# Optimization experiments

Hardware: AMD Instinct MI355X
Metric: run time of the kernel (lower is better)

## Reference

```python
import jax, jax.numpy as jnp
import numpy as np

LENGTH = 512
Q = 2 * LENGTH + 3   # match + insert + flank/unannotated/terminal states
S = 26               # amino-acid alphabet size


def setup_inputs() -> dict:
    key = jax.random.key(0)
    k1, k2, k3, k4 = jax.random.split(key, 4)
    seq = jax.random.randint(k1, (256, 512), 0, S, dtype=jnp.int32)
    A_logits = jax.random.normal(k2, (Q, Q), dtype=jnp.float32)
    B_logits = jax.random.normal(k3, (Q, S), dtype=jnp.float32)
    init_logits = jax.random.normal(k4, (Q,), dtype=jnp.float32)
    return {"seq": seq, "A_logits": A_logits, "B_logits": B_logits,
            "init_logits": init_logits}


def reference(seq, A_logits, B_logits, init_logits):
    # Row-stochastic transition matrix A [q,q], emission matrix B [q,s],
    # initial state distribution init [q] (cell builds these from kernels
    # via softmax/normalization in make_A()/make_B()).
    A = jax.nn.softmax(A_logits, axis=-1)
    B = jax.nn.softmax(B_logits, axis=-1)
    init = jax.nn.softmax(init_logits)

    # Emission likelihoods per timestep: E[b,t,q] = B[q, seq[b,t]]
    E = B.T[seq]  # [batch, T, q]

    # Scaled HMM forward recursion (log-sum-exp in scaled prob space).
    alpha0 = init[None, :] * E[:, 0]            # [batch, q]
    s0 = jnp.sum(alpha0, axis=-1)               # [batch]
    carry0 = (alpha0 / s0[:, None], jnp.log(s0))

    def step(carry, e_t):
        alpha, ll = carry
        f = (alpha @ A) * e_t                   # [batch, q]
        s = jnp.sum(f, axis=-1)                 # scaling factor
        return (f / s[:, None], ll + jnp.log(s)), None

    E_rest = jnp.transpose(E[:, 1:], (1, 0, 2))  # [T-1, batch, q]
    (alpha, loglik), _ = jax.lax.scan(step, carry0, E_rest)
    return loglik  # per-sequence log-likelihood [batch]
```

## Files before the change

kernel.cpp:

```cpp
#include <hip/hip_runtime.h>
#include <math.h>

typedef __bf16 bf16x8 __attribute__((ext_vector_type(8)));
typedef float f32x4 __attribute__((ext_vector_type(4)));
typedef unsigned int u32x4 __attribute__((ext_vector_type(4)));
typedef unsigned long long u64;

constexpr int QQ = 1027;
constexpr int SS = 26;
constexpr int TT = 512;
constexpr int NB = 256;
constexpr int KP = 1056;
constexpr int NP = 1040;
constexpr int BTS = 1040;
constexpr int NSL = 13;
constexpr int NBB = 16;
constexpr int MB = 16;
constexpr int NWV = 5;
constexpr int CBLK = NWV * 64;
constexpr int KSTEPS = KP / 32;
constexpr int BUFN = NB * KP;
constexpr int RQ = KP / 4;
constexpr int LQ = 274;
constexpr int TOTQ = MB * RQ;
constexpr int NLD = TOTQ / CBLK;
constexpr int NREM = TOTQ - NLD * CBLK;
constexpr int NTAG = NSL * NWV;
constexpr int TSTR = 80;

__device__ __forceinline__ unsigned short f2bf(float f) {
  union { float f; unsigned u; } v; v.f = f;
  return (unsigned short)((v.u + 0x7fffu + ((v.u >> 16) & 1u)) >> 16);
}

__device__ __forceinline__ u64 ald8(const u64* p) {
  return __hip_atomic_load((u64*)p, __ATOMIC_RELAXED, __HIP_MEMORY_SCOPE_AGENT);
}
__device__ __forceinline__ void ast8(u64* p, u64 v) {
  __hip_atomic_store(p, v, __ATOMIC_RELAXED, __HIP_MEMORY_SCOPE_AGENT);
}

__device__ __forceinline__ void spin_tag(const u64* p, unsigned texp) {
  u64 v = ald8(p);
  while ((unsigned)(v >> 32) != texp) {
    __builtin_amdgcn_s_sleep(1);
    v = ald8(p);
  }
}

__device__ __forceinline__ float sum4bf(u64 q) {
  union { unsigned u; float f; } a, b, c, d;
  a.u = ((unsigned)(q & 0xFFFFu)) << 16;
  b.u = (unsigned)(q >> 16) << 16;
  b.u = ((unsigned)((q >> 16) & 0xFFFFu)) << 16;
  c.u = ((unsigned)((q >> 32) & 0xFFFFu)) << 16;
  d.u = ((unsigned)((q >> 48) & 0xFFFFu)) << 16;
  return (a.f + b.f) + (c.f + d.f);
}

__global__ void k_zero(u32x4* p, int n) {
  int i = blockIdx.x * blockDim.x + threadIdx.x;
  if (i < n) p[i] = (u32x4){0u, 0u, 0u, 0u};
}

__global__ void k_prep_init(const float* __restrict__ il, float* __restrict__ ip) {
  __shared__ float red[1024];
  int tid = threadIdx.x;
  float m = -1e30f;
  for (int q = tid; q < QQ; q += 1024) m = fmaxf(m, il[q]);
  red[tid] = m; __syncthreads();
  for (int off = 512; off > 0; off >>= 1) {
    if (tid < off) red[tid] = fmaxf(red[tid], red[tid + off]);
    __syncthreads();
  }
  m = red[0]; __syncthreads();
  float s = 0.f;
  for (int q = tid; q < QQ; q += 1024) s += expf(il[q] - m);
  red[tid] = s; __syncthreads();
  for (int off = 512; off > 0; off >>= 1) {
    if (tid < off) red[tid] += red[tid + off];
    __syncthreads();
  }
  s = red[0];
  float inv = 1.0f / s;
  for (int q = tid; q < QQ; q += 1024) ip[q] = expf(il[q] - m) * inv;
}

__global__ void k_prep_B(const float* __restrict__ bl, float* __restrict__ bt) {
  int q = blockIdx.x * blockDim.x + threadIdx.x;
  if (q >= QQ) return;
  const float* row = bl + (size_t)q * SS;
  float m = -1e30f;
  for (int c = 0; c < SS; ++c) m = fmaxf(m, row[c]);
  float s = 0.f;
  for (int c = 0; c < SS; ++c) s += expf(row[c] - m);
  float inv = 1.0f / s;
  for (int c = 0; c < SS; ++c) bt[c * BTS + q] = expf(row[c] - m) * inv;
}

__global__ void k_prep_A(const float* __restrict__ al, unsigned short* __restrict__ at) {
  int r = blockIdx.x;
  const float* row = al + (size_t)r * QQ;
  __shared__ float red[256];
  int tid = threadIdx.x;
  float m = -1e30f;
  for (int n = tid; n < QQ; n += 256) m = fmaxf(m, row[n]);
  red[tid] = m; __syncthreads();
  for (int off = 128; off > 0; off >>= 1) {
    if (tid < off) red[tid] = fmaxf(red[tid], red[tid + off]);
    __syncthreads();
  }
  m = red[0]; __syncthreads();
  float s = 0.f;
  for (int n = tid; n < QQ; n += 256) s += expf(row[n] - m);
  red[tid] = s; __syncthreads();
  for (int off = 128; off > 0; off >>= 1) {
    if (tid < off) red[tid] += red[tid + off];
    __syncthreads();
  }
  s = red[0];
  float inv = 1.0f / s;
  for (int n = tid; n < QQ; n += 256) at[(size_t)n * KP + r] = f2bf(expf(row[n] - m) * inv);
}

__global__ void k_init_step(const int* __restrict__ seq, const float* __restrict__ ip,
                            const float* __restrict__ Bt, unsigned short* __restrict__ buf0) {
  int b = blockIdx.x, tid = threadIdx.x;
  int c0 = seq[b * TT];
  for (int q = tid; q < NP; q += 256)
    buf0[(size_t)b * KP + q] = f2bf(ip[q] * Bt[c0 * BTS + q]);
}

__global__ __launch_bounds__(CBLK, 1) void k_hmm_coop(
    const int* __restrict__ seq, const unsigned short* __restrict__ At,
    const float* __restrict__ Bt, unsigned short* __restrict__ bufB,
    u64* __restrict__ tagsE, float* __restrict__ out) {
  __shared__ u64 aldsq[MB * LQ];
  __shared__ float srowF[MB];

  const int tid = threadIdx.x, wg = blockIdx.x;
  const int bb = wg % NBB, sl = wg / NBB;
  const int lane = tid & 63, wv = tid >> 6;
  const int lrow = lane >> 4, lcol = lane & 15;
  const int n0w = (sl * NWV + wv) * 16;

  u32x4 atr[KSTEPS];
  {
    const u32x4* atp = (const u32x4*)(At + (size_t)(n0w + lcol) * KP + 8 * lrow);
#pragma unroll
    for (int ks = 0; ks < KSTEPS; ++ks) atr[ks] = atp[4 * ks];
  }
  const u32x4 ones4 = (u32x4){0x3F803F80u, 0x3F803F80u, 0x3F803F80u, 0x3F803F80u};

  float ll = 0.f;

  for (int t = 1; t < TT; ++t) {
    const int rd = (t - 1) % 3, wri = t % 3;
    const unsigned texp = (unsigned)(t - 1);
    const u64* tagb = tagsE + ((size_t)rd * NBB + bb) * TSTR;
    u64* tagw = tagsE + ((size_t)wri * NBB + bb) * TSTR;
    const u64* ain = (const u64*)(bufB + (size_t)rd * BUFN) + (size_t)bb * TOTQ;
    u64* wbuf8 = (u64*)(bufB + (size_t)wri * BUFN);

    const int ch = seq[(bb * MB + lcol) * TT + t];
    const f32x4 ev = *(const f32x4*)(Bt + (size_t)ch * BTS + n0w + 4 * lrow);

    if (tid < NTAG) spin_tag(tagb + tid, texp);
    __syncthreads();

    u64 av[NLD], avx = 0;
    const u64* asrc = ain + tid;
#pragma unroll
    for (int j = 0; j < NLD; ++j) av[j] = ald8(asrc + j * CBLK);
    if (tid < NREM) avx = ald8(asrc + NLD * CBLK);

#pragma unroll
    for (int j = 0; j < NLD; ++j) {
      int g = tid + j * CBLK;
      int r = g / RQ;
      aldsq[r * LQ + (g - r * RQ)] = av[j];
    }
    if (tid < NREM) {
      int g = tid + NLD * CBLK;
      int r = g / RQ;
      aldsq[r * LQ + (g - r * RQ)] = avx;
    }
    __syncthreads();

    const u32x4* ap = ((const u32x4*)aldsq) + lcol * (LQ / 2) + lrow;
    f32x4 acc = (f32x4){0.f, 0.f, 0.f, 0.f};
    f32x4 accs = (f32x4){0.f, 0.f, 0.f, 0.f};
#pragma unroll
    for (int ks = 0; ks < KSTEPS; ++ks) {
      u32x4 af = ap[4 * ks];
      acc = __builtin_amdgcn_mfma_f32_16x16x32_bf16(
          __builtin_bit_cast(bf16x8, atr[ks]), __builtin_bit_cast(bf16x8, af),
          acc, 0, 0, 0);
      accs = __builtin_amdgcn_mfma_f32_16x16x32_bf16(
          __builtin_bit_cast(bf16x8, ones4), __builtin_bit_cast(bf16x8, af),
          accs, 0, 0, 0);
    }

    const float s = accs[0];
    const float inv = 1.0f / s;
    if (sl == 0 && wv == 0) ll += logf(s);

    u64 hv = 0;
#pragma unroll
    for (int i = 0; i < 4; ++i) {
      float v = acc[i] * ev[i] * inv;
      hv |= (u64)f2bf(v) << (16 * i);
    }
    ast8(wbuf8 + (size_t)(bb * MB + lcol) * RQ + (n0w >> 2) + lrow, hv);
    asm volatile("s_waitcnt vmcnt(0)" ::: "memory");
    if (lane == 0) ast8(tagw + sl * NWV + wv, (u64)(unsigned)t << 32);
  }

  if (sl == 0) {
    if (tid < MB) srowF[tid] = 0.f;
    const int fs = (TT - 1) % 3;
    const u64* tagb = tagsE + ((size_t)fs * NBB + bb) * TSTR;
    if (tid < NTAG) spin_tag(tagb + tid, (unsigned)(TT - 1));
    __syncthreads();
    const u64* ain = (const u64*)(bufB + (size_t)fs * BUFN) + (size_t)bb * TOTQ;
#pragma unroll
    for (int j = 0; j < NLD; ++j) {
      int g = tid + j * CBLK;
      atomicAdd(&srowF[g / RQ], sum4bf(ald8(ain + g)));
    }
    if (tid < NREM) {
      int g = tid + NLD * CBLK;
      atomicAdd(&srowF[g / RQ], sum4bf(ald8(ain + g)));
    }
    __syncthreads();
    if (wv == 0 && lrow == 0) out[bb * MB + lcol] = ll + logf(srowF[lcol]);
  }
}

extern "C" void kernel_launch(void* const* d_in, const int* in_sizes, int n_in,
                              void* d_out, int out_size, void* d_ws, size_t ws_size,
                              hipStream_t stream) {
  const int* seq = (const int*)d_in[0];
  const float* Al = (const float*)d_in[1];
  const float* Bl = (const float*)d_in[2];
  const float* il = (const float*)d_in[3];
  float* out = (float*)d_out;

  char* ws = (char*)d_ws;
  unsigned short* At = (unsigned short*)ws;
  size_t off_bt = (size_t)NP * KP * 2;
  float* Bt = (float*)(ws + off_bt);
  size_t off_ip = off_bt + (size_t)SS * BTS * 4;
  float* ip = (float*)(ws + off_ip);
  size_t off_buf = off_ip + (size_t)NP * 4;
  unsigned short* bufB = (unsigned short*)(ws + off_buf);
  size_t off_tag = off_buf + (size_t)3 * BUFN * 2;
  u64* tagsE = (u64*)(ws + off_tag);
  size_t total = off_tag + (size_t)3 * NBB * TSTR * 8;
  int n16 = (int)((total + 15) / 16);

  k_zero<<<(n16 + 255) / 256, 256, 0, stream>>>((u32x4*)ws, n16);
  k_prep_init<<<1, 1024, 0, stream>>>(il, ip);
  k_prep_B<<<(QQ + 255) / 256, 256, 0, stream>>>(Bl, Bt);
  k_prep_A<<<QQ, 256, 0, stream>>>(Al, At);
  k_init_step<<<NB, 256, 0, stream>>>(seq, ip, Bt, bufB);

  void* args[] = {(void*)&seq, (void*)&At, (void*)&Bt, (void*)&bufB,
                  (void*)&tagsE, (void*)&out};
  hipLaunchCooperativeKernel((void*)k_hmm_coop, dim3(NBB * NSL), dim3(CBLK),
                             args, 0, stream);
}
```

Before: 1.625 ms.

## Replace per-step tag flags with parity bits embedded in bf16 data words

Drops the separate tag array and its spin-waits. Each stored bf16 now carries a parity bit in its sign bit, marking which timestep wrote it. Readers poll the data words directly until the parity matches, then mask off the sign bits. This removes the s_waitcnt-then-flag-store round trip and the tag-poll-then-load latency on every step. In exchange, a buffer is prefilled with sign bits, the row stride is compacted to NP, and correctness depends on each 8-byte store and load being atomic and on all probabilities being non-negative.

```diff
diff --git a/kernel.cpp b/kernel.cpp
--- a/kernel.cpp
+++ b/kernel.cpp
@@ -19,14 +19,12 @@
 constexpr int NWV = 5;
 constexpr int CBLK = NWV * 64;
 constexpr int KSTEPS = KP / 32;
-constexpr int BUFN = NB * KP;
-constexpr int RQ = KP / 4;
+constexpr int BUFN = NB * NP;
+constexpr int BSQ = NP / 4;
 constexpr int LQ = 274;
-constexpr int TOTQ = MB * RQ;
+constexpr int TOTQ = MB * BSQ;
 constexpr int NLD = TOTQ / CBLK;
-constexpr int NREM = TOTQ - NLD * CBLK;
-constexpr int NTAG = NSL * NWV;
-constexpr int TSTR = 80;
+constexpr u64 SMASK = 0x7FFF7FFF7FFF7FFFull;
 
 __device__ __forceinline__ unsigned short f2bf(float f) {
   union { float f; unsigned u; } v; v.f = f;
@@ -40,18 +38,18 @@
   __hip_atomic_store(p, v, __ATOMIC_RELAXED, __HIP_MEMORY_SCOPE_AGENT);
 }
 
-__device__ __forceinline__ void spin_tag(const u64* p, unsigned texp) {
-  u64 v = ald8(p);
-  while ((unsigned)(v >> 32) != texp) {
+__device__ __forceinline__ u64 poll_word(const u64* p, unsigned par, u64 first) {
+  u64 v = first;
+  while ((unsigned)((v >> 15) & 1ull) != par) {
     __builtin_amdgcn_s_sleep(1);
     v = ald8(p);
   }
+  return v;
 }
 
 __device__ __forceinline__ float sum4bf(u64 q) {
   union { unsigned u; float f; } a, b, c, d;
   a.u = ((unsigned)(q & 0xFFFFu)) << 16;
-  b.u = (unsigned)(q >> 16) << 16;
   b.u = ((unsigned)((q >> 16) & 0xFFFFu)) << 16;
   c.u = ((unsigned)((q >> 32) & 0xFFFFu)) << 16;
   d.u = ((unsigned)((q >> 48) & 0xFFFFu)) << 16;
@@ -61,6 +59,11 @@
 __global__ void k_zero(u32x4* p, int n) {
   int i = blockIdx.x * blockDim.x + threadIdx.x;
   if (i < n) p[i] = (u32x4){0u, 0u, 0u, 0u};
+}
+
+__global__ void k_fill(u32x4* p, int n) {
+  int i = blockIdx.x * blockDim.x + threadIdx.x;
+  if (i < n) p[i] = (u32x4){0x80008000u, 0x80008000u, 0x80008000u, 0x80008000u};
 }
 
 __global__ void k_prep_init(const float* __restrict__ il, float* __restrict__ ip) {
@@ -128,13 +131,13 @@
   int b = blockIdx.x, tid = threadIdx.x;
   int c0 = seq[b * TT];
   for (int q = tid; q < NP; q += 256)
-    buf0[(size_t)b * KP + q] = f2bf(ip[q] * Bt[c0 * BTS + q]);
+    buf0[(size_t)b * NP + q] = f2bf(ip[q] * Bt[c0 * BTS + q]);
 }
 
 __global__ __launch_bounds__(CBLK, 1) void k_hmm_coop(
     const int* __restrict__ seq, const unsigned short* __restrict__ At,
     const float* __restrict__ Bt, unsigned short* __restrict__ bufB,
-    u64* __restrict__ tagsE, float* __restrict__ out) {
+    float* __restrict__ out) {
   __shared__ u64 aldsq[MB * LQ];
   __shared__ float srowF[MB];
 
@@ -144,6 +147,8 @@
   const int lrow = lane >> 4, lcol = lane & 15;
   const int n0w = (sl * NWV + wv) * 16;
 
+  if (tid < 64) aldsq[(tid >> 2) * LQ + 260 + (tid & 3)] = 0;
+
   u32x4 atr[KSTEPS];
   {
     const u32x4* atp = (const u32x4*)(At + (size_t)(n0w + lcol) * KP + 8 * lrow);
@@ -156,34 +161,27 @@
 
   for (int t = 1; t < TT; ++t) {
     const int rd = (t - 1) % 3, wri = t % 3;
-    const unsigned texp = (unsigned)(t - 1);
-    const u64* tagb = tagsE + ((size_t)rd * NBB + bb) * TSTR;
-    u64* tagw = tagsE + ((size_t)wri * NBB + bb) * TSTR;
+    const unsigned par = (unsigned)((t - 1) & 1);
+    const u64 wtag = (u64)(unsigned)(t & 1) << 15;
     const u64* ain = (const u64*)(bufB + (size_t)rd * BUFN) + (size_t)bb * TOTQ;
     u64* wbuf8 = (u64*)(bufB + (size_t)wri * BUFN);
 
     const int ch = seq[(bb * MB + lcol) * TT + t];
     const f32x4 ev = *(const f32x4*)(Bt + (size_t)ch * BTS + n0w + 4 * lrow);
 
-    if (tid < NTAG) spin_tag(tagb + tid, texp);
-    __syncthreads();
-
-    u64 av[NLD], avx = 0;
+    u64 av[NLD];
     const u64* asrc = ain + tid;
 #pragma unroll
     for (int j = 0; j < NLD; ++j) av[j] = ald8(asrc + j * CBLK);
-    if (tid < NREM) avx = ald8(asrc + NLD * CBLK);
+#pragma unroll
+    for (int j = 0; j < NLD; ++j)
+      av[j] = poll_word(asrc + j * CBLK, par, av[j]) & SMASK;
 
 #pragma unroll
     for (int j = 0; j < NLD; ++j) {
       int g = tid + j * CBLK;
-      int r = g / RQ;
-      aldsq[r * LQ + (g - r * RQ)] = av[j];
-    }
-    if (tid < NREM) {
-      int g = tid + NLD * CBLK;
-      int r = g / RQ;
-      aldsq[r * LQ + (g - r * RQ)] = avx;
+      int r = g / BSQ;
+      aldsq[r * LQ + (g - r * BSQ)] = av[j];
     }
     __syncthreads();
 
@@ -209,28 +207,23 @@
 #pragma unroll
     for (int i = 0; i < 4; ++i) {
       float v = acc[i] * ev[i] * inv;
-      hv |= (u64)f2bf(v) << (16 * i);
-    }
-    ast8(wbuf8 + (size_t)(bb * MB + lcol) * RQ + (n0w >> 2) + lrow, hv);
-    asm volatile("s_waitcnt vmcnt(0)" ::: "memory");
-    if (lane == 0) ast8(tagw + sl * NWV + wv, (u64)(unsigned)t << 32);
+      hv |= ((u64)f2bf(v) | wtag) << (16 * i);
+    }
+    ast8(wbuf8 + (size_t)(bb * MB + lcol) * BSQ + (n0w >> 2) + lrow, hv);
+    __syncthreads();
   }
 
   if (sl == 0) {
     if (tid < MB) srowF[tid] = 0.f;
+    __syncthreads();
     const int fs = (TT - 1) % 3;
-    const u64* tagb = tagsE + ((size_t)fs * NBB + bb) * TSTR;
-    if (tid < NTAG) spin_tag(tagb + tid, (unsigned)(TT - 1));
-    __syncthreads();
+    const unsigned parF = (unsigned)((TT - 1) & 1);
     const u64* ain = (const u64*)(bufB + (size_t)fs * BUFN) + (size_t)bb * TOTQ;
 #pragma unroll
     for (int j = 0; j < NLD; ++j) {
       int g = tid + j * CBLK;
-      atomicAdd(&srowF[g / RQ], sum4bf(ald8(ain + g)));
-    }
-    if (tid < NREM) {
-      int g = tid + NLD * CBLK;
-      atomicAdd(&srowF[g / RQ], sum4bf(ald8(ain + g)));
+      u64 q = poll_word(ain + g, parF, ald8(ain + g)) & SMASK;
+      atomicAdd(&srowF[g / BSQ], sum4bf(q));
     }
     __syncthreads();
     if (wv == 0 && lrow == 0) out[bb * MB + lcol] = ll + logf(srowF[lcol]);
@@ -254,19 +247,19 @@
   float* ip = (float*)(ws + off_ip);
   size_t off_buf = off_ip + (size_t)NP * 4;
   unsigned short* bufB = (unsigned short*)(ws + off_buf);
-  size_t off_tag = off_buf + (size_t)3 * BUFN * 2;
-  u64* tagsE = (u64*)(ws + off_tag);
-  size_t total = off_tag + (size_t)3 * NBB * TSTR * 8;
+  size_t total = off_buf + (size_t)3 * BUFN * 2;
   int n16 = (int)((total + 15) / 16);
 
   k_zero<<<(n16 + 255) / 256, 256, 0, stream>>>((u32x4*)ws, n16);
+  int nf = (int)(((size_t)BUFN * 2) / 16);
+  k_fill<<<(nf + 255) / 256, 256, 0, stream>>>(
+      (u32x4*)(bufB + (size_t)2 * BUFN), nf);
   k_prep_init<<<1, 1024, 0, stream>>>(il, ip);
   k_prep_B<<<(QQ + 255) / 256, 256, 0, stream>>>(Bl, Bt);
   k_prep_A<<<QQ, 256, 0, stream>>>(Al, At);
   k_init_step<<<NB, 256, 0, stream>>>(seq, ip, Bt, bufB);
 
-  void* args[] = {(void*)&seq, (void*)&At, (void*)&Bt, (void*)&bufB,
-                  (void*)&tagsE, (void*)&out};
+  void* args[] = {(void*)&seq, (void*)&At, (void*)&Bt, (void*)&bufB, (void*)&out};
   hipLaunchCooperativeKernel((void*)k_hmm_coop, dim3(NBB * NSL), dim3(CBLK),
                              args, 0, stream);
 }
```

After: 1.926 ms. 18.5% more time.
